# Kernel optimization log

Measured on AMD Instinct MI355X. Metric: run time of the kernel, lower is better.

## Reference

```python
import jax, jax.numpy as jnp
import numpy as np

TWO_PI = 2.0 * np.pi


def setup_inputs() -> dict:
    key = jax.random.key(0)
    k1, k2 = jax.random.split(key)
    # positions: [batch=1, N=1024 patches, D=2 spatial axes], values in [0,1)
    positions = jax.random.uniform(k1, (1, 1024, 2), dtype=jnp.float32)
    # learned generator params: [D=2, L=4 layers, G=128 generators, g=8, g=8]
    gen_params = jax.random.uniform(k2, (2, 4, 128, 8, 8), dtype=jnp.float32) * TWO_PI
    return {"positions": positions, "gen_params": gen_params}


def reference(positions, gen_params):
    # phase_type == 'learned' branch
    # upper triangle (strictly above diagonal) shifted by -0.5; the shift
    # cancels in the skew-symmetrization, matching the torch code exactly.
    upper = jnp.triu(gen_params, k=1) - 0.5
    bases = upper - jnp.swapaxes(upper, -1, -2)  # skew-symmetric [D,L,G,g,g]
    # position-weighted sum over spatial axes D: [1,N,L,G,g,g]
    gen_pos = jnp.einsum('bnd,dlgij->bnlgij', positions, bases)
    # prepend zero generator for the cls token -> identity rotation
    cls = jnp.zeros_like(gen_pos[:, :1])
    gen_pos = jnp.concatenate([cls, gen_pos], axis=1)  # [1,N+1,L,G,g,g]
    # batched matrix exponential of tiny 8x8 skew-symmetric matrices
    shape = gen_pos.shape
    g = shape[-1]
    rot = jax.vmap(jax.scipy.linalg.expm)(
        gen_pos.astype(jnp.float32).reshape(-1, g, g)
    ).reshape(shape)
    return rot
```

## Files before the change

### kernel.cpp

```cpp
#include <hip/hip_runtime.h>
#include <cstdint>

constexpr int LG   = 512;
constexpr int NPOS = 1025;
constexpr int NMAT = NPOS * LG;
constexpr int GEN_ELEMS = 2 * LG * 64;

__host__ __device__ constexpr int UI(int i, int j) { return i*7 - (i*(i-1))/2 + (j - i - 1); }
__host__ __device__ constexpr int SI(int i, int j) { return i*8 - (i*(i-1))/2 + (j - i); }

#define YSsym(a,b)  Ys [ (a)<=(b) ? SI(a,b) : SI(b,a) ]
#define Y2sym(a,b)  Y2s[ (a)<=(b) ? SI(a,b) : SI(b,a) ]
#define EEsym(a,b)  Zs [ (a)<=(b) ? SI(a,b) : SI(b,a) ]
#define OOsym(a,b)  Y2s[ (a)<=(b) ? SI(a,b) : SI(b,a) ]
#define XV(i,k) ( (i)<(k) ? U[UI(i,k)] : -U[UI(k,i)] )

__device__ __forceinline__ void sq64(float (&D)[64], const float (&S)[64]) {
    #pragma unroll
    for (int i = 0; i < 8; ++i)
        #pragma unroll
        for (int j = 0; j < 8; ++j) {
            float acc = S[i*8+0] * S[0*8+j];
            #pragma unroll
            for (int k = 1; k < 8; ++k)
                acc = fmaf(S[i*8+k], S[k*8+j], acc);
            D[i*8+j] = acc;
        }
}

__global__ __launch_bounds__(256)
void liere_tr_kernel(const float* __restrict__ g, float* __restrict__ gT) {
    int t = blockIdx.x * 256 + threadIdx.x;
    if (t >= GEN_ELEMS) return;
    int d  = t >> 15;
    int lg = (t >> 6) & 511;
    int e  = t & 63;
    gT[(size_t)e * 1024 + lg * 2 + d] = g[t];
}

template<bool TR>
__global__ __launch_bounds__(256)
void liere_expm_kernel(const float* __restrict__ pos,
                       const float* __restrict__ gen,
                       const float* __restrict__ genT,
                       float* __restrict__ out)
{
    const int bid = blockIdx.x, tid = threadIdx.x;
    const int n   = bid >> 1;
    const int lg  = ((bid & 1) << 8) | tid;

    float P[64];

    if (n == 0) {
        #pragma unroll
        for (int i = 0; i < 8; ++i)
            #pragma unroll
            for (int j = 0; j < 8; ++j)
                P[i*8+j] = (i == j) ? 1.f : 0.f;
    } else {
        const float p0 = pos[(n-1)*2 + 0];
        const float p1 = pos[(n-1)*2 + 1];

        float U[28];
        if (TR) {
            #pragma unroll
            for (int i = 0; i < 8; ++i)
                #pragma unroll
                for (int j = i+1; j < 8; ++j) {
                    const int e = i*8 + j;
                    float2 v = *reinterpret_cast<const float2*>(
                                   genT + (size_t)e * 1024 + lg * 2);
                    U[UI(i,j)] = fmaf(p0, v.x, p1 * v.y);
                }
        } else {
            const float* g0 = gen + (size_t)lg * 64;
            const float* g1 = g0 + (size_t)LG * 64;
            #pragma unroll
            for (int i = 0; i < 8; ++i)
                #pragma unroll
                for (int j = i+1; j < 8; ++j) {
                    const int e = i*8 + j;
                    U[UI(i,j)] = fmaf(p0, g0[e], p1 * g1[e]);
                }
        }

        float Ys[36];
        #pragma unroll
        for (int i = 0; i < 8; ++i)
            #pragma unroll
            for (int j = i; j < 8; ++j) {
                float acc = 0.f;
                #pragma unroll
                for (int k = 0; k < 8; ++k) {
                    if (k == i || k == j) continue;
                    acc = fmaf(XV(i,k), XV(k,j), acc);
                }
                Ys[SI(i,j)] = acc;
            }

        float Y2s[36];
        #pragma unroll
        for (int i = 0; i < 8; ++i)
            #pragma unroll
            for (int j = i; j < 8; ++j) {
                float acc = YSsym(i,0) * YSsym(0,j);
                #pragma unroll
                for (int k = 1; k < 8; ++k)
                    acc = fmaf(YSsym(i,k), YSsym(k,j), acc);
                Y2s[SI(i,j)] = acc;
            }

        float trY = 0.f;
        #pragma unroll
        for (int i = 0; i < 8; ++i) trY += Ys[SI(i,i)];
        float dYY=0.f, oYY=0.f, dY3=0.f, oY3=0.f, d44=0.f, o44=0.f;
        #pragma unroll
        for (int i = 0; i < 8; ++i)
            #pragma unroll
            for (int j = i; j < 8; ++j) {
                float y = Ys[SI(i,j)], y2 = Y2s[SI(i,j)];
                if (i == j) { dYY=fmaf(y,y,dYY); dY3=fmaf(y,y2,dY3); d44=fmaf(y2,y2,d44); }
                else        { oYY=fmaf(y,y,oYY); oY3=fmaf(y,y2,oY3); o44=fmaf(y2,y2,o44); }
            }
        const float sYY = fmaf(2.f, oYY, dYY);
        const float sY3 = fmaf(2.f, oY3, dY3);
        const float s44 = fmaf(2.f, o44, d44);

        float yb = 0.f;
        #pragma unroll
        for (int i = 0; i < 8; ++i) {
            float rs = fabsf(Y2sym(i,0));
            #pragma unroll
            for (int j = 1; j < 8; ++j) rs += fabsf(Y2sym(i,j));
            yb = fmaxf(yb, rs);
        }
        float q4 = fmaxf(fminf(yb, 0.5f * s44), 1e-30f);
        int r = (int)ceilf(0.25f * __log2f(q4) - 3.0f);
        if (r < 0) r = 0;
        if (r > 5) r = 5;

        const float r1 = __uint_as_float((uint32_t)(127 - r) << 23);
        const float r2 = r1 * r1;
        const float r4 = r2 * r2;
        #pragma unroll
        for (int k = 0; k < 28; ++k) U[k]   *= r1;
        #pragma unroll
        for (int k = 0; k < 36; ++k) Ys[k]  *= r2;
        #pragma unroll
        for (int k = 0; k < 36; ++k) Y2s[k] *= r4;

        const double R2 = (double)r2;
        const double R4 = R2 * R2;
        const double P1 = -0.5 * (double)trY * R2;
        const double P2 =  0.5 * (double)sYY * R4;
        const double P3 = -0.5 * (double)sY3 * R4 * R2;
        const double P4 =  0.5 * (double)s44 * R4 * R4;
        const double E1 = P1;
        const double E2 = 0.5 * (E1*P1 - P2);
        const double E3 = (1.0/3.0) * (E2*P1 - E1*P2 + P3);
        const double E4 = 0.25 * (E3*P1 - E2*P2 + E1*P3 - P4);

        double c[37];
        c[0] = 1.0;
        #pragma unroll
        for (int k = 1; k <= 36; ++k) c[k] = c[k-1] / (double)k;
        #pragma unroll
        for (int d = 36; d >= 8; --d) {
            double t = c[d];
            c[d-2] = fma(-E1, t, c[d-2]);
            c[d-4] = fma(-E2, t, c[d-4]);
            c[d-6] = fma(-E3, t, c[d-6]);
            c[d-8] = fma(-E4, t, c[d-8]);
        }
        float cf[8];
        #pragma unroll
        for (int k = 0; k < 8; ++k) cf[k] = (float)c[k];

        float Zs[36];
        #pragma unroll
        for (int i = 0; i < 8; ++i)
            #pragma unroll
            for (int j = i; j < 8; ++j) {
                float acc = YSsym(i,0) * Y2sym(0,j);
                #pragma unroll
                for (int k = 1; k < 8; ++k)
                    acc = fmaf(YSsym(i,k), Y2sym(k,j), acc);
                Zs[SI(i,j)] = acc;
            }

        #pragma unroll
        for (int k = 0; k < 36; ++k) {
            float y = Ys[k], y2 = Y2s[k], z = Zs[k];
            Zs[k]  = fmaf(cf[6], z, fmaf(cf[4], y2, cf[2]*y));
            Y2s[k] = fmaf(cf[7], z, fmaf(cf[5], y2, cf[3]*y));
        }
        #pragma unroll
        for (int i = 0; i < 8; ++i) {
            Zs[SI(i,i)]  += cf[0];
            Y2s[SI(i,i)] += cf[1];
        }

        #pragma unroll
        for (int i = 0; i < 8; ++i)
            #pragma unroll
            for (int j = 0; j < 8; ++j) {
                float acc = EEsym(i,j);
                #pragma unroll
                for (int k = 0; k < 8; ++k) {
                    if (k == i) continue;
                    acc = fmaf(XV(i,k), OOsym(k,j), acc);
                }
                P[i*8+j] = acc;
            }

        for (int t = 0; t < r; ++t) {
            float Q[64];
            sq64(Q, P);
            #pragma unroll
            for (int k = 0; k < 64; ++k) P[k] = Q[k];
        }
    }

    __shared__ float4 ls[256 * 8];
    float4* o4base = reinterpret_cast<float4*>(out) + (size_t)bid * 4096;
    #pragma unroll
    for (int rr = 0; rr < 2; ++rr) {
        if (rr) __syncthreads();
        #pragma unroll
        for (int j = 0; j < 8; ++j) {
            const int jj = rr*8 + j;
            ls[tid*8 + ((j + tid) & 7)] =
                make_float4(P[4*jj+0], P[4*jj+1], P[4*jj+2], P[4*jj+3]);
        }
        __syncthreads();
        #pragma unroll
        for (int k = 0; k < 8; ++k) {
            const int u = k*256 + tid;
            const int o = u >> 3, cidx = u & 7;
            o4base[o*16 + cidx + 8*rr] = ls[o*8 + ((cidx + o) & 7)];
        }
    }
}

extern "C" void kernel_launch(void* const* d_in, const int* in_sizes, int n_in,
                              void* d_out, int out_size, void* d_ws, size_t ws_size,
                              hipStream_t stream) {
    const float* pos = (const float*)d_in[0];
    const float* gen = (const float*)d_in[1];
    float* out = (float*)d_out;

    const int block = 256;
    const int grid  = NMAT / block;

    if (ws_size >= (size_t)GEN_ELEMS * sizeof(float)) {
        float* genT = (float*)d_ws;
        liere_tr_kernel<<<GEN_ELEMS / 256, 256, 0, stream>>>(gen, genT);
        liere_expm_kernel<true><<<grid, block, 0, stream>>>(pos, gen, genT, out);
    } else {
        liere_expm_kernel<false><<<grid, block, 0, stream>>>(pos, gen, nullptr, out);
    }
}
```

Before: 53.81 us.

## Fold scaling into polynomial coefficients, precompute factorials, pair squarings, wave-uniform r

Stops scaling the U, Y and Y2 matrices element by element and folds the power-of-two scale into the eight polynomial coefficients instead. The factorial table becomes a constant array and the characteristic-polynomial reduction is truncated from 36 to 30 terms. The squaring count is reduced to its maximum across the 64-lane wave, so all lanes take the same branch, and squarings run in ping-pong pairs to avoid register copies. Lanes with small norms may now do extra squarings, and the shorter series could slightly change accuracy for large arguments.

```diff
diff --git a/kernel.cpp b/kernel.cpp
--- a/kernel.cpp
+++ b/kernel.cpp
@@ -135,21 +135,14 @@
             yb = fmaxf(yb, rs);
         }
         float q4 = fmaxf(fminf(yb, 0.5f * s44), 1e-30f);
+        #pragma unroll
+        for (int off = 32; off >= 1; off >>= 1)
+            q4 = fmaxf(q4, __shfl_xor(q4, off, 64));
         int r = (int)ceilf(0.25f * __log2f(q4) - 3.0f);
         if (r < 0) r = 0;
         if (r > 5) r = 5;
 
-        const float r1 = __uint_as_float((uint32_t)(127 - r) << 23);
-        const float r2 = r1 * r1;
-        const float r4 = r2 * r2;
-        #pragma unroll
-        for (int k = 0; k < 28; ++k) U[k]   *= r1;
-        #pragma unroll
-        for (int k = 0; k < 36; ++k) Ys[k]  *= r2;
-        #pragma unroll
-        for (int k = 0; k < 36; ++k) Y2s[k] *= r4;
-
-        const double R2 = (double)r2;
+        const double R2 = (double)__uint_as_float((uint32_t)(127 - 2*r) << 23);
         const double R4 = R2 * R2;
         const double P1 = -0.5 * (double)trY * R2;
         const double P2 =  0.5 * (double)sYY * R4;
@@ -160,21 +153,31 @@
         const double E3 = (1.0/3.0) * (E2*P1 - E1*P2 + P3);
         const double E4 = 0.25 * (E3*P1 - E2*P2 + E1*P3 - P4);
 
-        double c[37];
-        c[0] = 1.0;
-        #pragma unroll
-        for (int k = 1; k <= 36; ++k) c[k] = c[k-1] / (double)k;
-        #pragma unroll
-        for (int d = 36; d >= 8; --d) {
+        double c[31] = {
+            1.0, 1.0, 0.5, 0.16666666666666666, 0.041666666666666664,
+            0.008333333333333333, 0.001388888888888889, 1.984126984126984e-4,
+            2.48015873015873e-5, 2.7557319223985893e-6, 2.755731922398589e-7,
+            2.505210838544172e-8, 2.08767569878681e-9, 1.6059043836821613e-10,
+            1.1470745597729725e-11, 7.647163731819816e-13, 4.779477332387385e-14,
+            2.8114572543455206e-15, 1.5619206968586225e-16, 8.22063524662433e-18,
+            4.110317623312165e-19, 1.9572941063391263e-20, 8.896791392450574e-22,
+            3.868170170630684e-23, 1.6117375710961184e-24, 6.446950284384474e-26,
+            2.4795962632247976e-27, 9.183689863795546e-29, 3.279889237069838e-30,
+            1.1309962886447716e-31, 3.7699876288159054e-33
+        };
+        #pragma unroll
+        for (int d = 30; d >= 8; --d) {
             double t = c[d];
             c[d-2] = fma(-E1, t, c[d-2]);
             c[d-4] = fma(-E2, t, c[d-4]);
             c[d-6] = fma(-E3, t, c[d-6]);
             c[d-8] = fma(-E4, t, c[d-8]);
         }
+        const double W = (double)__uint_as_float((uint32_t)(127 - r) << 23);
+        double wk = 1.0;
         float cf[8];
         #pragma unroll
-        for (int k = 0; k < 8; ++k) cf[k] = (float)c[k];
+        for (int k = 0; k < 8; ++k) { cf[k] = (float)(c[k] * wk); wk *= W; }
 
         float Zs[36];
         #pragma unroll
@@ -213,11 +216,15 @@
                 P[i*8+j] = acc;
             }
 
-        for (int t = 0; t < r; ++t) {
+        {
             float Q[64];
-            sq64(Q, P);
-            #pragma unroll
-            for (int k = 0; k < 64; ++k) P[k] = Q[k];
+            int pairs = r >> 1;
+            while (pairs--) { sq64(Q, P); sq64(P, Q); }
+            if (r & 1) {
+                sq64(Q, P);
+                #pragma unroll
+                for (int t = 0; t < 64; ++t) P[t] = Q[t];
+            }
         }
     }
 
```

Measured after the change: 51.64 us. 4.0% less time.
